# Performance work log

Hardware: AMD Instinct MI355X
Metric: run time of the kernel (lower is better)

Reference implementation:

```python
import jax, jax.numpy as jnp
import numpy as np

D_MODEL = 1024
NUM_HEADS = 16
HEAD_DIM = 64
INNER = NUM_HEADS * HEAD_DIM


def setup_inputs() -> dict:
    key = jax.random.key(0)
    k_x, k_q, k_k, k_v, k_o = jax.random.split(key, 5)
    B, T = 4, 2048
    s = 1.0 / np.sqrt(D_MODEL)
    return {
        "x": jax.random.normal(k_x, (B, T, D_MODEL), dtype=jnp.float32),
        "W_q": jax.random.uniform(k_q, (D_MODEL, INNER), dtype=jnp.float32, minval=-s, maxval=s),
        "W_k": jax.random.uniform(k_k, (D_MODEL, INNER), dtype=jnp.float32, minval=-s, maxval=s),
        "W_v": jax.random.uniform(k_v, (D_MODEL, INNER), dtype=jnp.float32, minval=-s, maxval=s),
        "W_o": jax.random.uniform(k_o, (INNER, D_MODEL), dtype=jnp.float32, minval=-s, maxval=s),
    }


def reference(x, W_q, W_k, W_v, W_o):
    B, T, _ = x.shape
    scale = HEAD_DIM ** -0.5
    # project and split heads: [B, H, T, Dh]
    q = (x @ W_q).reshape(B, T, NUM_HEADS, HEAD_DIM).transpose(0, 2, 1, 3)
    k = (x @ W_k).reshape(B, T, NUM_HEADS, HEAD_DIM).transpose(0, 2, 1, 3)
    v = (x @ W_v).reshape(B, T, NUM_HEADS, HEAD_DIM).transpose(0, 2, 1, 3)
    scores = jnp.einsum("bhqd,bhkd->bhqk", q, k) * scale  # [B,H,T,T]
    causal = jnp.tril(jnp.ones((T, T), dtype=bool))
    scores = jnp.where(causal, scores, -jnp.inf)
    probs = jax.nn.softmax(scores, axis=-1)
    ctx = jnp.einsum("bhqk,bhkd->bhqd", probs, v)
    ctx = ctx.transpose(0, 2, 1, 3).reshape(B, T, INNER)
    return ctx @ W_o
```

## Files before the change

### kernel.cpp

```cpp
#include <hip/hip_runtime.h>


typedef short  short8  __attribute__((ext_vector_type(8)));
typedef short  short4v __attribute__((ext_vector_type(4)));
typedef float  floatx4 __attribute__((ext_vector_type(4)));
typedef unsigned uint2v __attribute__((ext_vector_type(2)));

#define T_SZ 2048
#define DM   1024

#define QSCALE 0.18033688011112042f

__device__ __forceinline__ short f2bf(float f) {
  unsigned u = __float_as_uint(f);
  u += 0x7fffu + ((u >> 16) & 1u);
  return (short)(u >> 16);
}

#if defined(__has_builtin) && __has_builtin(__builtin_amdgcn_cvt_pk_bf16_f32)
typedef __bf16 bf16x2_t __attribute__((ext_vector_type(2)));
__device__ __forceinline__ unsigned pack_bf(float lo, float hi) {
  return __builtin_bit_cast(unsigned, __builtin_amdgcn_cvt_pk_bf16_f32(lo, hi));
}
#else
__device__ __forceinline__ unsigned pack_bf(float lo, float hi) {
  return __builtin_amdgcn_perm(__float_as_uint(hi) + 0x8000u,
                               __float_as_uint(lo) + 0x8000u, 0x07060302u);
}
#endif

#if defined(__has_builtin) && __has_builtin(__builtin_amdgcn_exp2f)
__device__ __forceinline__ float fexp2(float x) { return __builtin_amdgcn_exp2f(x); }
#else
__device__ __forceinline__ float fexp2(float x) { return exp2f(x); }
#endif

__device__ __forceinline__ void gll16(const void* g, void* l) {
  __builtin_amdgcn_global_load_lds((const __attribute__((address_space(1))) void*)g,
                                   (__attribute__((address_space(3))) void*)l, 16, 0, 0);
}

__global__ void cvt_kernel(const float* __restrict__ s0, const float* __restrict__ s1,
                           const float* __restrict__ s2, const float* __restrict__ s3,
                           short* __restrict__ dst,
                           const float* __restrict__ x, short* __restrict__ xb) {
  const int tx = threadIdx.x, ty = threadIdx.y;
  if (blockIdx.z == 4) {
    const int tid = ty * 32 + tx;
    const int blk = blockIdx.y * 32 + blockIdx.x;
    int i = (blk * 256 + tid) * 4;
#pragma unroll
    for (int j = 0; j < 8; ++j) {
      const float4 v = *(const float4*)(x + i);
      short4v o;
      o.x = f2bf(v.x); o.y = f2bf(v.y); o.z = f2bf(v.z); o.w = f2bf(v.w);
      *(short4v*)(xb + i) = o;
      i += 1048576;
    }
    return;
  }
  const float* srcs[4] = {s0, s1, s2, s3};
  const float* src = srcs[blockIdx.z];
  short* d = dst + (size_t)blockIdx.z * 1048576;
  __shared__ float tile[32][33];
  const int n_base = blockIdx.x * 32, k_base = blockIdx.y * 32;
#pragma unroll
  for (int j = 0; j < 4; ++j)
    tile[ty + j * 8][tx] = src[(size_t)(k_base + ty + j * 8) * 1024 + n_base + tx];
  __syncthreads();
#pragma unroll
  for (int j = 0; j < 4; ++j)
    d[(size_t)(n_base + ty + j * 8) * 1024 + k_base + tx] = f2bf(tile[tx][ty + j * 8]);
}

template <int MODE>
__global__ void gemm_bt(const short* __restrict__ A, const short* __restrict__ Bt,
                        short* __restrict__ obf, short* __restrict__ vt,
                        float* __restrict__ of, int K) {
  __shared__ short As[128 * 32];
  __shared__ short Bs[128 * 32];
  const int tid  = threadIdx.x;
  const int w    = tid >> 6, lane = tid & 63;
  const int quad = lane >> 4, l15 = lane & 15;
  const int wr   = w >> 1, wc = w & 1;
  const int lid  = (int)blockIdx.y * 64 + (int)blockIdx.x;
  const int m0   = (((lid & 7) + 8 * ((lid >> 3) & 7))) * 128;
  const int n0   = (lid >> 6) * 128;
  const int arow = tid >> 2, apart = tid & 3;

  floatx4 acc[4][4] = {};

  for (int kk = 0; kk < K; kk += 32) {
    gll16(A  + (size_t)(m0 + arow) * K      + kk + apart * 8, &As[tid * 8]);
    gll16(A  + (size_t)(m0 + 64 + arow) * K + kk + apart * 8, &As[(256 + tid) * 8]);
    gll16(Bt + (size_t)(n0 + arow) * K      + kk + apart * 8, &Bs[tid * 8]);
    gll16(Bt + (size_t)(n0 + 64 + arow) * K + kk + apart * 8, &Bs[(256 + tid) * 8]);
    __syncthreads();
    short8 af[4], bf[4];
#pragma unroll
    for (int i = 0; i < 4; ++i)
      af[i] = *(const short8*)&As[(wr * 64 + i * 16 + l15) * 32 + quad * 8];
#pragma unroll
    for (int j = 0; j < 4; ++j)
      bf[j] = *(const short8*)&Bs[(wc * 64 + j * 16 + l15) * 32 + quad * 8];
#pragma unroll
    for (int i = 0; i < 4; ++i)
#pragma unroll
      for (int j = 0; j < 4; ++j)
        acc[i][j] = __builtin_amdgcn_mfma_f32_16x16x32_bf16(af[i], bf[j], acc[i][j], 0, 0, 0);
    __syncthreads();
  }

  if (MODE == 0) {
    const int wsel = n0 >> 10;
    const int ncol0 = (n0 & 1023) + wc * 64;
    if (wsel < 2) {
      const float scale = (wsel == 0) ? QSCALE : 1.0f;
      short* outw = obf + (size_t)wsel * (64u * 2048u * 64u);
#pragma unroll
      for (int i = 0; i < 4; ++i) {
        const int row0 = m0 + wr * 64 + i * 16 + quad * 4;
#pragma unroll
        for (int j = 0; j < 4; ++j) {
          const int col = ncol0 + j * 16 + l15;
          const int h = col >> 6, d = col & 63;
#pragma unroll
          for (int r = 0; r < 4; ++r) {
            const int rg = row0 + r;
            const int b = rg >> 11, t = rg & 2047;
            outw[(((size_t)(b * 16 + h) * 2048 + t) << 6) + d] = f2bf(acc[i][j][r] * scale);
          }
        }
      }
    } else {
#pragma unroll
      for (int i = 0; i < 4; ++i) {
        const int row0 = m0 + wr * 64 + i * 16 + quad * 4;
        const int b = row0 >> 11, t = row0 & 2047;
#pragma unroll
        for (int j = 0; j < 4; ++j) {
          const int col = ncol0 + j * 16 + l15;
          const int h = col >> 6, d = col & 63;
          short4v pv;
#pragma unroll
          for (int r = 0; r < 4; ++r) pv[r] = f2bf(acc[i][j][r]);
          *(short4v*)(vt + (((size_t)(b * 16 + h) * 64 + d) << 11) + t) = pv;
        }
      }
    }
  } else {
#pragma unroll
    for (int i = 0; i < 4; ++i) {
      const int row0 = m0 + wr * 64 + i * 16 + quad * 4;
#pragma unroll
      for (int j = 0; j < 4; ++j) {
        const int col = n0 + wc * 64 + j * 16 + l15;
#pragma unroll
        for (int r = 0; r < 4; ++r)
          of[(size_t)(row0 + r) * 1024 + col] = acc[i][j][r];
      }
    }
  }
}

__global__ __launch_bounds__(256, 2) void attn_kernel(
    const short* __restrict__ Qg, const short* __restrict__ Kg,
    const short* __restrict__ Vt, short* __restrict__ ctx) {
  __shared__ short Ks[128 * 72];
  __shared__ short Vs[80 * 132];
  __shared__ short Ps[4 * 32 * 136];

  const int tid  = threadIdx.x;
  const int w    = tid >> 6, lane = tid & 63;
  const int quad = lane >> 4, l15 = lane & 15;
  const int bh = (int)blockIdx.x + 8 * ((int)blockIdx.y & 7);
  const int p  = (int)blockIdx.y >> 3;
  const int b  = bh >> 4, h = bh & 15;

  const size_t base = (size_t)bh * (T_SZ * 64);
  const short* Qb  = Qg + base;
  const short* Kb  = Kg + base;
  const short* Vtb = Vt + base;
  short* Pw = &Ps[w * (32 * 136)];

  const int skr = tid >> 1, skc = (tid & 1) * 32;
  const int svr = tid >> 2, svc = (tid & 3) * 32;

  {
    const int rr = 64 + (tid >> 4), cb = (tid & 15) * 8;
    const short vv = (tid < 16) ? (short)0x3F80 : (short)0;
    short8 fill;
#pragma unroll
    for (int j = 0; j < 8; ++j) fill[j] = vv;
    *(short8*)&Vs[rr * 132 + cb] = fill;
  }

  for (int qsel = 0; qsel < 2; ++qsel) {
    const int qi = qsel ? (15 - p) : p;
    const int q0 = qi << 7;
    const int rowA = q0 + w * 32;
    const int rowB = rowA + 16;

    const short8 qA0 = *(const short8*)(Qb + (size_t)(rowA + l15) * 64 + quad * 8);
    const short8 qA1 = *(const short8*)(Qb + (size_t)(rowA + l15) * 64 + 32 + quad * 8);
    const short8 qB0 = *(const short8*)(Qb + (size_t)(rowB + l15) * 64 + quad * 8);
    const short8 qB1 = *(const short8*)(Qb + (size_t)(rowB + l15) * 64 + 32 + quad * 8);

    floatx4 OA[4] = {}, OB[4] = {};
    floatx4 O5A = {}, O5B = {};

    const int ktiles = qi + 1;
    short8 kR[4], vR[4];
#pragma unroll
    for (int j = 0; j < 4; ++j) {
      kR[j] = *(const short8*)(Kb + (size_t)skr * 64 + skc + j * 8);
      vR[j] = *(const short8*)(Vtb + (size_t)svr * 2048 + svc + j * 8);
    }

    for (int kt = 0; kt < ktiles; ++kt) {
      const int k0 = kt << 7;
      __syncthreads();
#pragma unroll
      for (int j = 0; j < 4; ++j) {
        *(short8*)&Ks[skr * 72 + skc + j * 8] = kR[j];
        *(short8*)&Vs[svr * 132 + svc + j * 8] = vR[j];
      }
      if (kt + 1 < ktiles) {
        const int kn = (kt + 1) << 7;
#pragma unroll
        for (int j = 0; j < 4; ++j) {
          kR[j] = *(const short8*)(Kb + (size_t)(kn + skr) * 64 + skc + j * 8);
          vR[j] = *(const short8*)(Vtb + (size_t)svr * 2048 + kn + svc + j * 8);
        }
      }
      __syncthreads();

      const int dkA = rowA - k0;
      const int dkB = dkA + 16;
      const int limA = dkA + l15, limB = limA + 16;
      const int naA = min(8, (dkA >> 4) + 1), nchA = (naA + 1) >> 1;
      const int naB = min(8, (dkB >> 4) + 1), nchB = (naB + 1) >> 1;

#pragma unroll
      for (int mt = 0; mt < 8; ++mt) {
        const int pa = l15 * 136 + mt * 16 + quad * 4;
        const int pb = (16 + l15) * 136 + mt * 16 + quad * 4;
        const bool actA = (mt * 16 < dkA + 16);
        const bool actB = (mt * 16 < dkB + 16);
        if (actB) {
          const short8 kf0 = *(const short8*)&Ks[(mt * 16 + l15) * 72 + quad * 8];
          const short8 kf1 = *(const short8*)&Ks[(mt * 16 + l15) * 72 + 32 + quad * 8];
          {
            floatx4 s = {};
            s = __builtin_amdgcn_mfma_f32_16x16x32_bf16(kf0, qB0, s, 0, 0, 0);
            s = __builtin_amdgcn_mfma_f32_16x16x32_bf16(kf1, qB1, s, 0, 0, 0);
            if (mt * 16 + 15 > dkB) {
#pragma unroll
              for (int r = 0; r < 4; ++r)
                if (mt * 16 + quad * 4 + r > limB) s[r] = -1e30f;
            }
            floatx4 e;
#pragma unroll
            for (int r = 0; r < 4; ++r) e[r] = fexp2(s[r]);
            uint2v pd;
            pd.x = pack_bf(e[0], e[1]);
            pd.y = pack_bf(e[2], e[3]);
            *(uint2v*)&Pw[pb] = pd;
          }
          if (actA) {
            floatx4 s = {};
            s = __builtin_amdgcn_mfma_f32_16x16x32_bf16(kf0, qA0, s, 0, 0, 0);
            s = __builtin_amdgcn_mfma_f32_16x16x32_bf16(kf1, qA1, s, 0, 0, 0);
            if (mt * 16 + 15 > dkA) {
#pragma unroll
              for (int r = 0; r < 4; ++r)
                if (mt * 16 + quad * 4 + r > limA) s[r] = -1e30f;
            }
            floatx4 e;
#pragma unroll
            for (int r = 0; r < 4; ++r) e[r] = fexp2(s[r]);
            uint2v pd;
            pd.x = pack_bf(e[0], e[1]);
            pd.y = pack_bf(e[2], e[3]);
            *(uint2v*)&Pw[pa] = pd;
          } else if (mt < 2 * nchA) {
            uint2v z; z.x = 0; z.y = 0;
            *(uint2v*)&Pw[pa] = z;
          }
        } else {
          uint2v z; z.x = 0; z.y = 0;
          if (mt < 2 * nchB) *(uint2v*)&Pw[pb] = z;
          if (mt < 2 * nchA) *(uint2v*)&Pw[pa] = z;
        }
      }

#pragma unroll
      for (int c = 0; c < 4; ++c) {
        if (c < nchB) {
          const short8 vfl = *(const short8*)&Vs[(64 + l15) * 132 + c * 32 + quad * 8];
          short8 vf[4];
#pragma unroll
          for (int dt = 0; dt < 4; ++dt)
            vf[dt] = *(const short8*)&Vs[(dt * 16 + l15) * 132 + c * 32 + quad * 8];
          const short8 pfB = *(const short8*)&Pw[(16 + l15) * 136 + c * 32 + quad * 8];
#pragma unroll
          for (int dt = 0; dt < 4; ++dt)
            OB[dt] = __builtin_amdgcn_mfma_f32_16x16x32_bf16(vf[dt], pfB, OB[dt], 0, 0, 0);
          O5B = __builtin_amdgcn_mfma_f32_16x16x32_bf16(vfl, pfB, O5B, 0, 0, 0);
          if (c < nchA) {
            const short8 pfA = *(const short8*)&Pw[l15 * 136 + c * 32 + quad * 8];
#pragma unroll
            for (int dt = 0; dt < 4; ++dt)
              OA[dt] = __builtin_amdgcn_mfma_f32_16x16x32_bf16(vf[dt], pfA, OA[dt], 0, 0, 0);
            O5A = __builtin_amdgcn_mfma_f32_16x16x32_bf16(vfl, pfA, O5A, 0, 0, 0);
          }
        }
      }
    }

    {
      const float lA = __shfl(O5A[0], l15);
      const float invA = 1.0f / lA;
      const int t = rowA + l15;
      short* cb = ctx + (((size_t)(b * T_SZ + t)) << 10) + h * 64 + quad * 4;
#pragma unroll
      for (int dt = 0; dt < 4; ++dt) {
        short4v o4;
#pragma unroll
        for (int r = 0; r < 4; ++r) o4[r] = f2bf(OA[dt][r] * invA);
        *(short4v*)(cb + dt * 16) = o4;
      }
    }
    {
      const float lB = __shfl(O5B[0], l15);
      const float invB = 1.0f / lB;
      const int t = rowB + l15;
      short* cb = ctx + (((size_t)(b * T_SZ + t)) << 10) + h * 64 + quad * 4;
#pragma unroll
      for (int dt = 0; dt < 4; ++dt) {
        short4v o4;
#pragma unroll
        for (int r = 0; r < 4; ++r) o4[r] = f2bf(OB[dt][r] * invB);
        *(short4v*)(cb + dt * 16) = o4;
      }
    }
  }
}

extern "C" void kernel_launch(void* const* d_in, const int* in_sizes, int n_in,
                              void* d_out, int out_size, void* d_ws, size_t ws_size,
                              hipStream_t stream) {
  const float* x  = (const float*)d_in[0];
  const float* Wq = (const float*)d_in[1];
  const float* Wk = (const float*)d_in[2];
  const float* Wv = (const float*)d_in[3];
  const float* Wo = (const float*)d_in[4];
  float* out = (float*)d_out;

  short* ws  = (short*)d_ws;
  short* xb  = ws;
  short* Wt  = ws + 8388608;
  short* Qb  = Wt + 4 * 1048576;
  short* Kb  = Qb + 8388608;
  short* Vt  = Kb + 8388608;
  short* ctx = xb;

  cvt_kernel<<<dim3(32, 32, 5), dim3(32, 8), 0, stream>>>(Wq, Wk, Wv, Wo, Wt, x, xb);
  gemm_bt<0><<<dim3(64, 24), 256, 0, stream>>>(xb, Wt, Qb, Vt, nullptr, 1024);
  attn_kernel<<<dim3(8, 64), 256, 0, stream>>>(Qb, Kb, Vt, ctx);
  gemm_bt<1><<<dim3(64, 8), 256, 0, stream>>>(ctx, Wt + 3 * 1048576, nullptr, nullptr, out, 1024);
}
```

Measured before the change: 256.6 us.

## Add 256x256-tile pipelined QKV GEMM with swizzled LDS and double buffering

Replaces the generic 128x128 single-buffered QKV projection GEMM with a dedicated 512-thread kernel using 256x256 tiles, a BK=64 double-buffered LDS pipeline fed by direct global-to-LDS loads, XOR-swizzled LDS layout, and interleaved MFMA quadrants with manual waitcnt/barrier and setprio scheduling. It aims to cut global traffic through larger reuse, hide load latency behind MFMAs, and avoid LDS bank conflicts. The 128KB of LDS per block and fewer blocks (384) reduce occupancy, and the hand-written waitcnt sequencing risks subtle races.

```diff
diff --git a/kernel.cpp b/kernel.cpp
--- a/kernel.cpp
+++ b/kernel.cpp
@@ -39,6 +39,11 @@
   __builtin_amdgcn_global_load_lds((const __attribute__((address_space(1))) void*)g,
                                    (__attribute__((address_space(3))) void*)l, 16, 0, 0);
 }
+
+#define SBAR() asm volatile("s_barrier" ::: "memory")
+#define WLG()  asm volatile("s_waitcnt lgkmcnt(0)" ::: "memory")
+#define WV6()  asm volatile("s_waitcnt vmcnt(6)" ::: "memory")
+#define WV0()  asm volatile("s_waitcnt vmcnt(0)" ::: "memory")
 
 __global__ void cvt_kernel(const float* __restrict__ s0, const float* __restrict__ s1,
                            const float* __restrict__ s2, const float* __restrict__ s3,
@@ -71,6 +76,139 @@
 #pragma unroll
   for (int j = 0; j < 4; ++j)
     d[(size_t)(n_base + ty + j * 8) * 1024 + k_base + tx] = f2bf(tile[tx][ty + j * 8]);
+}
+
+__global__ __launch_bounds__(512, 2) void gemm_qkv(
+    const short* __restrict__ A, const short* __restrict__ Bt,
+    short* __restrict__ obf, short* __restrict__ vt) {
+  __shared__ short As[32768];
+  __shared__ short Bs[32768];
+  const int tid  = threadIdx.x;
+  const int w    = tid >> 6, lane = tid & 63;
+  const int quad = lane >> 4, l15 = lane & 15;
+  const int wr   = w >> 2, wc = w & 3;
+  const int fx   = l15 & 7;
+  const int lid  = (int)blockIdx.x;
+  const int m0   = ((lid & 7) * 4 + ((lid >> 3) & 3)) * 256;
+  const int n0   = (lid >> 5) * 256;
+  const int srow = tid >> 3;
+  const int scol = ((tid & 7) ^ (srow & 7)) * 8;
+
+  const short* Ag = A  + (size_t)(m0 + srow) * 1024 + scol;
+  const short* Bg = Bt + (size_t)(n0 + srow) * 1024 + scol;
+  const short* Ab[2] = { &As[(0 * 2 + wr) * 8192], &As[(1 * 2 + wr) * 8192] };
+  const short* Bb[2] = { &Bs[(0 * 2 + (wc >> 1)) * 8192], &Bs[(1 * 2 + (wc >> 1)) * 8192] };
+  const int br0 = (wc & 1) * 64;
+
+  floatx4 acc[8][4] = {};
+  short8 af[4][2], bf[4][2];
+
+#define STG_A(slot, h, kb) do { \
+    short* _lb = &As[((slot) * 2 + (h)) * 8192 + tid * 8]; \
+    const short* _gp = Ag + (size_t)(h) * (128 * 1024) + (kb); \
+    gll16(_gp, _lb); \
+    gll16(_gp + (size_t)(64 * 1024), _lb + 4096); \
+  } while (0)
+#define STG_B(slot, h, kb) do { \
+    short* _lb = &Bs[((slot) * 2 + (h)) * 8192 + tid * 8]; \
+    const short* _gp = Bg + (size_t)(h) * (128 * 1024) + (kb); \
+    gll16(_gp, _lb); \
+    gll16(_gp + (size_t)(64 * 1024), _lb + 4096); \
+  } while (0)
+#define LDA4(slot, ih) do { \
+    _Pragma("unroll") for (int ii = 0; ii < 4; ++ii) \
+    _Pragma("unroll") for (int s = 0; s < 2; ++s) \
+      af[ii][s] = *(const short8*)&Ab[slot][(((ih) * 4 + ii) * 16 + l15) * 64 + (((s * 4 + quad) ^ fx)) * 8]; \
+  } while (0)
+#define LDB8(slot) do { \
+    _Pragma("unroll") for (int j = 0; j < 4; ++j) \
+    _Pragma("unroll") for (int s = 0; s < 2; ++s) \
+      bf[j][s] = *(const short8*)&Bb[slot][(br0 + j * 16 + l15) * 64 + (((s * 4 + quad) ^ fx)) * 8]; \
+  } while (0)
+#define MMQ(ih, jh) do { \
+    __builtin_amdgcn_s_setprio(1); \
+    _Pragma("unroll") for (int ii = 0; ii < 4; ++ii) \
+    _Pragma("unroll") for (int jj = 0; jj < 2; ++jj) \
+    _Pragma("unroll") for (int s = 0; s < 2; ++s) \
+      acc[(ih) * 4 + ii][(jh) * 2 + jj] = __builtin_amdgcn_mfma_f32_16x16x32_bf16( \
+          af[ii][s], bf[(jh) * 2 + jj][s], acc[(ih) * 4 + ii][(jh) * 2 + jj], 0, 0, 0); \
+    __builtin_amdgcn_s_setprio(0); \
+  } while (0)
+
+  STG_A(0, 0, 0);  STG_A(0, 1, 0);
+  STG_B(0, 0, 0);  STG_B(0, 1, 0);
+  STG_B(1, 0, 64); STG_B(1, 1, 64);
+  STG_A(1, 0, 64);
+  WV6(); SBAR();
+
+  for (int t = 0; t < 8; ++t) {
+    const int kp1 = (2 * t + 1) * 64;
+    const int kn2 = (2 * t + 2) * 64;
+    const int kn3 = (2 * t + 3) * 64;
+    const bool mre = (t < 7);
+    LDA4(0, 0); LDB8(0);
+    STG_A(1, 1, kp1);
+    SBAR(); WLG(); MMQ(0, 0); SBAR();
+    if (mre) STG_B(0, 0, kn2);
+    SBAR(); MMQ(0, 1); SBAR();
+    LDA4(0, 1);
+    if (mre) STG_B(0, 1, kn2);
+    SBAR(); WLG(); MMQ(1, 0); SBAR();
+    if (mre) { STG_A(0, 0, kn2); WV6(); } else { WV0(); }
+    SBAR(); MMQ(1, 1); SBAR();
+    LDA4(1, 0); LDB8(1);
+    if (mre) STG_A(0, 1, kn2);
+    SBAR(); WLG(); MMQ(0, 0); SBAR();
+    if (mre) STG_B(1, 0, kn3);
+    SBAR(); MMQ(0, 1); SBAR();
+    LDA4(1, 1);
+    if (mre) STG_B(1, 1, kn3);
+    SBAR(); WLG(); MMQ(1, 0); SBAR();
+    if (mre) { STG_A(1, 0, kn3); WV6(); }
+    SBAR(); MMQ(1, 1); SBAR();
+  }
+
+  const int wsel  = n0 >> 10;
+  const int ncol0 = (n0 & 1023) + wc * 64;
+  if (wsel < 2) {
+    const float scale = (wsel == 0) ? QSCALE : 1.0f;
+    short* outw = obf + (size_t)wsel * (64u * 2048u * 64u);
+#pragma unroll
+    for (int i = 0; i < 8; ++i) {
+      const int row0 = m0 + wr * 128 + i * 16 + quad * 4;
+#pragma unroll
+      for (int j = 0; j < 4; ++j) {
+        const int col = ncol0 + j * 16 + l15;
+        const int h = col >> 6, d = col & 63;
+#pragma unroll
+        for (int r = 0; r < 4; ++r) {
+          const int rg = row0 + r;
+          const int b = rg >> 11, tt = rg & 2047;
+          outw[(((size_t)(b * 16 + h) * 2048 + tt) << 6) + d] = f2bf(acc[i][j][r] * scale);
+        }
+      }
+    }
+  } else {
+#pragma unroll
+    for (int i = 0; i < 8; ++i) {
+      const int row0 = m0 + wr * 128 + i * 16 + quad * 4;
+      const int b = row0 >> 11, tt = row0 & 2047;
+#pragma unroll
+      for (int j = 0; j < 4; ++j) {
+        const int col = ncol0 + j * 16 + l15;
+        const int h = col >> 6, d = col & 63;
+        short4v pv;
+#pragma unroll
+        for (int r = 0; r < 4; ++r) pv[r] = f2bf(acc[i][j][r]);
+        *(short4v*)(vt + (((size_t)(b * 16 + h) * 64 + d) << 11) + tt) = pv;
+      }
+    }
+  }
+#undef STG_A
+#undef STG_B
+#undef LDA4
+#undef LDB8
+#undef MMQ
 }
 
 template <int MODE>
@@ -96,18 +234,18 @@
     gll16(Bt + (size_t)(n0 + arow) * K      + kk + apart * 8, &Bs[tid * 8]);
     gll16(Bt + (size_t)(n0 + 64 + arow) * K + kk + apart * 8, &Bs[(256 + tid) * 8]);
     __syncthreads();
-    short8 af[4], bf[4];
+    short8 af[4], bfr[4];
 #pragma unroll
     for (int i = 0; i < 4; ++i)
       af[i] = *(const short8*)&As[(wr * 64 + i * 16 + l15) * 32 + quad * 8];
 #pragma unroll
     for (int j = 0; j < 4; ++j)
-      bf[j] = *(const short8*)&Bs[(wc * 64 + j * 16 + l15) * 32 + quad * 8];
+      bfr[j] = *(const short8*)&Bs[(wc * 64 + j * 16 + l15) * 32 + quad * 8];
 #pragma unroll
     for (int i = 0; i < 4; ++i)
 #pragma unroll
       for (int j = 0; j < 4; ++j)
-        acc[i][j] = __builtin_amdgcn_mfma_f32_16x16x32_bf16(af[i], bf[j], acc[i][j], 0, 0, 0);
+        acc[i][j] = __builtin_amdgcn_mfma_f32_16x16x32_bf16(af[i], bfr[j], acc[i][j], 0, 0, 0);
     __syncthreads();
   }
 
@@ -366,7 +504,7 @@
   short* ctx = xb;
 
   cvt_kernel<<<dim3(32, 32, 5), dim3(32, 8), 0, stream>>>(Wq, Wk, Wv, Wo, Wt, x, xb);
-  gemm_bt<0><<<dim3(64, 24), 256, 0, stream>>>(xb, Wt, Qb, Vt, nullptr, 1024);
+  gemm_qkv<<<dim3(384), 512, 0, stream>>>(xb, Wt, Qb, Vt);
   attn_kernel<<<dim3(8, 64), 256, 0, stream>>>(Qb, Kb, Vt, ctx);
   gemm_bt<1><<<dim3(64, 8), 256, 0, stream>>>(ctx, Wt + 3 * 1048576, nullptr, nullptr, out, 1024);
 }
```

Result: slower. 264.8 us (+3.2%).

## Restructure attention into 512-thread blocks over 256-row query tiles with chunked P

Applied to the files above, without the earlier changes.

The attention kernel now launches 512 threads (8 waves) per block. Each block covers one 256-row query tile, where before it processed two 128-row tiles in sequence to balance causal work. The tile order is reversed so the heaviest tiles start first. The probability scratch shrinks to a per-chunk 32x32 buffer per wave, with QK^T/exp and PV interleaved per 32-key chunk. Waves whose rows are entirely above the current key tile skip compute but still take part in the loads and barriers. This raises parallelism per block and lowers LDS use, but leaves some waves idle in the early key tiles.

```diff
diff --git a/kernel.cpp b/kernel.cpp
--- a/kernel.cpp
+++ b/kernel.cpp
@@ -96,18 +96,18 @@
     gll16(Bt + (size_t)(n0 + arow) * K      + kk + apart * 8, &Bs[tid * 8]);
     gll16(Bt + (size_t)(n0 + 64 + arow) * K + kk + apart * 8, &Bs[(256 + tid) * 8]);
     __syncthreads();
-    short8 af[4], bf[4];
+    short8 af[4], bfr[4];
 #pragma unroll
     for (int i = 0; i < 4; ++i)
       af[i] = *(const short8*)&As[(wr * 64 + i * 16 + l15) * 32 + quad * 8];
 #pragma unroll
     for (int j = 0; j < 4; ++j)
-      bf[j] = *(const short8*)&Bs[(wc * 64 + j * 16 + l15) * 32 + quad * 8];
+      bfr[j] = *(const short8*)&Bs[(wc * 64 + j * 16 + l15) * 32 + quad * 8];
 #pragma unroll
     for (int i = 0; i < 4; ++i)
 #pragma unroll
       for (int j = 0; j < 4; ++j)
-        acc[i][j] = __builtin_amdgcn_mfma_f32_16x16x32_bf16(af[i], bf[j], acc[i][j], 0, 0, 0);
+        acc[i][j] = __builtin_amdgcn_mfma_f32_16x16x32_bf16(af[i], bfr[j], acc[i][j], 0, 0, 0);
     __syncthreads();
   }
 
@@ -163,186 +163,184 @@
   }
 }
 
-__global__ __launch_bounds__(256, 2) void attn_kernel(
+__global__ __launch_bounds__(512, 4) void attn_kernel(
     const short* __restrict__ Qg, const short* __restrict__ Kg,
     const short* __restrict__ Vt, short* __restrict__ ctx) {
   __shared__ short Ks[128 * 72];
-  __shared__ short Vs[80 * 132];
-  __shared__ short Ps[4 * 32 * 136];
+  __shared__ short Vs[80 * 136];
+  __shared__ short Ps[8 * 32 * 40];
 
   const int tid  = threadIdx.x;
   const int w    = tid >> 6, lane = tid & 63;
   const int quad = lane >> 4, l15 = lane & 15;
   const int bh = (int)blockIdx.x + 8 * ((int)blockIdx.y & 7);
-  const int p  = (int)blockIdx.y >> 3;
+  const int g  = (int)blockIdx.y >> 3;
+  const int qb = (g < 4) ? (7 - g) : (g - 4);
   const int b  = bh >> 4, h = bh & 15;
 
   const size_t base = (size_t)bh * (T_SZ * 64);
   const short* Qb  = Qg + base;
   const short* Kb  = Kg + base;
   const short* Vtb = Vt + base;
-  short* Pw = &Ps[w * (32 * 136)];
-
-  const int skr = tid >> 1, skc = (tid & 1) * 32;
-  const int svr = tid >> 2, svc = (tid & 3) * 32;
-
-  {
+  short* Pw = &Ps[w * 1280];
+
+  const int skr = tid >> 2, skp = (tid & 3) * 16;
+  const int svr = tid >> 3, svp = (tid & 7) * 16;
+
+  if (tid < 256) {
     const int rr = 64 + (tid >> 4), cb = (tid & 15) * 8;
     const short vv = (tid < 16) ? (short)0x3F80 : (short)0;
     short8 fill;
 #pragma unroll
     for (int j = 0; j < 8; ++j) fill[j] = vv;
-    *(short8*)&Vs[rr * 132 + cb] = fill;
-  }
-
-  for (int qsel = 0; qsel < 2; ++qsel) {
-    const int qi = qsel ? (15 - p) : p;
-    const int q0 = qi << 7;
-    const int rowA = q0 + w * 32;
-    const int rowB = rowA + 16;
-
-    const short8 qA0 = *(const short8*)(Qb + (size_t)(rowA + l15) * 64 + quad * 8);
-    const short8 qA1 = *(const short8*)(Qb + (size_t)(rowA + l15) * 64 + 32 + quad * 8);
-    const short8 qB0 = *(const short8*)(Qb + (size_t)(rowB + l15) * 64 + quad * 8);
-    const short8 qB1 = *(const short8*)(Qb + (size_t)(rowB + l15) * 64 + 32 + quad * 8);
-
-    floatx4 OA[4] = {}, OB[4] = {};
-    floatx4 O5A = {}, O5B = {};
-
-    const int ktiles = qi + 1;
-    short8 kR[4], vR[4];
-#pragma unroll
-    for (int j = 0; j < 4; ++j) {
-      kR[j] = *(const short8*)(Kb + (size_t)skr * 64 + skc + j * 8);
-      vR[j] = *(const short8*)(Vtb + (size_t)svr * 2048 + svc + j * 8);
-    }
-
-    for (int kt = 0; kt < ktiles; ++kt) {
-      const int k0 = kt << 7;
-      __syncthreads();
-#pragma unroll
-      for (int j = 0; j < 4; ++j) {
-        *(short8*)&Ks[skr * 72 + skc + j * 8] = kR[j];
-        *(short8*)&Vs[svr * 132 + svc + j * 8] = vR[j];
-      }
-      if (kt + 1 < ktiles) {
-        const int kn = (kt + 1) << 7;
-#pragma unroll
-        for (int j = 0; j < 4; ++j) {
-          kR[j] = *(const short8*)(Kb + (size_t)(kn + skr) * 64 + skc + j * 8);
-          vR[j] = *(const short8*)(Vtb + (size_t)svr * 2048 + kn + svc + j * 8);
+    *(short8*)&Vs[rr * 136 + cb] = fill;
+  }
+
+  const int rowA = qb * 256 + w * 32;
+  const int rowB = rowA + 16;
+  const int ktmax = 2 * qb + 2;
+
+  const short8 qA0 = *(const short8*)(Qb + (size_t)(rowA + l15) * 64 + quad * 8);
+  const short8 qA1 = *(const short8*)(Qb + (size_t)(rowA + l15) * 64 + 32 + quad * 8);
+  const short8 qB0 = *(const short8*)(Qb + (size_t)(rowB + l15) * 64 + quad * 8);
+  const short8 qB1 = *(const short8*)(Qb + (size_t)(rowB + l15) * 64 + 32 + quad * 8);
+
+  floatx4 OA[4] = {}, OB[4] = {};
+  floatx4 O5A = {}, O5B = {};
+
+  short8 kR[2], vR[2];
+  kR[0] = *(const short8*)(Kb + (size_t)skr * 64 + skp);
+  kR[1] = *(const short8*)(Kb + (size_t)skr * 64 + skp + 8);
+  vR[0] = *(const short8*)(Vtb + (size_t)svr * 2048 + svp);
+  vR[1] = *(const short8*)(Vtb + (size_t)svr * 2048 + svp + 8);
+
+  for (int kt = 0; kt < ktmax; ++kt) {
+    const int k0 = kt << 7;
+    __syncthreads();
+    *(short8*)&Ks[skr * 72 + skp]     = kR[0];
+    *(short8*)&Ks[skr * 72 + skp + 8] = kR[1];
+    *(short8*)&Vs[svr * 136 + svp]     = vR[0];
+    *(short8*)&Vs[svr * 136 + svp + 8] = vR[1];
+    if (kt + 1 < ktmax) {
+      const int kn = (kt + 1) << 7;
+      kR[0] = *(const short8*)(Kb + (size_t)(kn + skr) * 64 + skp);
+      kR[1] = *(const short8*)(Kb + (size_t)(kn + skr) * 64 + skp + 8);
+      vR[0] = *(const short8*)(Vtb + (size_t)svr * 2048 + kn + svp);
+      vR[1] = *(const short8*)(Vtb + (size_t)svr * 2048 + kn + svp + 8);
+    }
+    __syncthreads();
+
+    const int dkA = rowA - k0;
+    if (dkA < 0) continue;
+    const int dkB = dkA + 16;
+    const int limA = dkA + l15, limB = limA + 16;
+    const int naA = min(8, (dkA >> 4) + 1), nchA = (naA + 1) >> 1;
+    const int naB = min(8, (dkB >> 4) + 1), nchB = (naB + 1) >> 1;
+
+#pragma unroll
+    for (int c = 0; c < 4; ++c) {
+      if (c < nchB) {
+#pragma unroll
+        for (int mm = 0; mm < 2; ++mm) {
+          const int mt = 2 * c + mm;
+          const int pa = l15 * 40 + mm * 16 + quad * 4;
+          const int pb = (16 + l15) * 40 + mm * 16 + quad * 4;
+          const bool aB = (mt * 16 < dkB + 16);
+          const bool aA = (mt * 16 < dkA + 16);
+          if (aB) {
+            const short8 kf0 = *(const short8*)&Ks[(mt * 16 + l15) * 72 + quad * 8];
+            const short8 kf1 = *(const short8*)&Ks[(mt * 16 + l15) * 72 + 32 + quad * 8];
+            {
+              floatx4 s = {};
+              s = __builtin_amdgcn_mfma_f32_16x16x32_bf16(kf0, qB0, s, 0, 0, 0);
+              s = __builtin_amdgcn_mfma_f32_16x16x32_bf16(kf1, qB1, s, 0, 0, 0);
+              if (mt * 16 + 15 > dkB) {
+#pragma unroll
+                for (int r = 0; r < 4; ++r)
+                  if (mt * 16 + quad * 4 + r > limB) s[r] = -1e30f;
+              }
+              floatx4 e;
+#pragma unroll
+              for (int r = 0; r < 4; ++r) e[r] = fexp2(s[r]);
+              uint2v pd;
+              pd.x = pack_bf(e[0], e[1]);
+              pd.y = pack_bf(e[2], e[3]);
+              *(uint2v*)&Pw[pb] = pd;
+            }
+            if (c < nchA) {
+              if (aA) {
+                floatx4 s = {};
+                s = __builtin_amdgcn_mfma_f32_16x16x32_bf16(kf0, qA0, s, 0, 0, 0);
+                s = __builtin_amdgcn_mfma_f32_16x16x32_bf16(kf1, qA1, s, 0, 0, 0);
+                if (mt * 16 + 15 > dkA) {
+#pragma unroll
+                  for (int r = 0; r < 4; ++r)
+                    if (mt * 16 + quad * 4 + r > limA) s[r] = -1e30f;
+                }
+                floatx4 e;
+#pragma unroll
+                for (int r = 0; r < 4; ++r) e[r] = fexp2(s[r]);
+                uint2v pd;
+                pd.x = pack_bf(e[0], e[1]);
+                pd.y = pack_bf(e[2], e[3]);
+                *(uint2v*)&Pw[pa] = pd;
+              } else {
+                uint2v z; z.x = 0; z.y = 0;
+                *(uint2v*)&Pw[pa] = z;
+              }
+            }
+          } else {
+            uint2v z; z.x = 0; z.y = 0;
+            *(uint2v*)&Pw[pb] = z;
+            if (c < nchA) *(uint2v*)&Pw[pa] = z;
+          }
+        }
+        const int vcol = c * 32 + quad * 8;
+        const short8 vfl = *(const short8*)&Vs[(64 + l15) * 136 + vcol];
+        short8 vf[4];
+#pragma unroll
+        for (int dt = 0; dt < 4; ++dt)
+          vf[dt] = *(const short8*)&Vs[(dt * 16 + l15) * 136 + vcol];
+        const short8 pfB = *(const short8*)&Pw[(16 + l15) * 40 + quad * 8];
+#pragma unroll
+        for (int dt = 0; dt < 4; ++dt)
+          OB[dt] = __builtin_amdgcn_mfma_f32_16x16x32_bf16(vf[dt], pfB, OB[dt], 0, 0, 0);
+        O5B = __builtin_amdgcn_mfma_f32_16x16x32_bf16(vfl, pfB, O5B, 0, 0, 0);
+        if (c < nchA) {
+          const short8 pfA = *(const short8*)&Pw[l15 * 40 + quad * 8];
+#pragma unroll
+          for (int dt = 0; dt < 4; ++dt)
+            OA[dt] = __builtin_amdgcn_mfma_f32_16x16x32_bf16(vf[dt], pfA, OA[dt], 0, 0, 0);
+          O5A = __builtin_amdgcn_mfma_f32_16x16x32_bf16(vfl, pfA, O5A, 0, 0, 0);
         }
       }
-      __syncthreads();
-
-      const int dkA = rowA - k0;
-      const int dkB = dkA + 16;
-      const int limA = dkA + l15, limB = limA + 16;
-      const int naA = min(8, (dkA >> 4) + 1), nchA = (naA + 1) >> 1;
-      const int naB = min(8, (dkB >> 4) + 1), nchB = (naB + 1) >> 1;
-
-#pragma unroll
-      for (int mt = 0; mt < 8; ++mt) {
-        const int pa = l15 * 136 + mt * 16 + quad * 4;
-        const int pb = (16 + l15) * 136 + mt * 16 + quad * 4;
-        const bool actA = (mt * 16 < dkA + 16);
-        const bool actB = (mt * 16 < dkB + 16);
-        if (actB) {
-          const short8 kf0 = *(const short8*)&Ks[(mt * 16 + l15) * 72 + quad * 8];
-          const short8 kf1 = *(const short8*)&Ks[(mt * 16 + l15) * 72 + 32 + quad * 8];
-          {
-            floatx4 s = {};
-            s = __builtin_amdgcn_mfma_f32_16x16x32_bf16(kf0, qB0, s, 0, 0, 0);
-            s = __builtin_amdgcn_mfma_f32_16x16x32_bf16(kf1, qB1, s, 0, 0, 0);
-            if (mt * 16 + 15 > dkB) {
-#pragma unroll
-              for (int r = 0; r < 4; ++r)
-                if (mt * 16 + quad * 4 + r > limB) s[r] = -1e30f;
-            }
-            floatx4 e;
-#pragma unroll
-            for (int r = 0; r < 4; ++r) e[r] = fexp2(s[r]);
-            uint2v pd;
-            pd.x = pack_bf(e[0], e[1]);
-            pd.y = pack_bf(e[2], e[3]);
-            *(uint2v*)&Pw[pb] = pd;
-          }
-          if (actA) {
-            floatx4 s = {};
-            s = __builtin_amdgcn_mfma_f32_16x16x32_bf16(kf0, qA0, s, 0, 0, 0);
-            s = __builtin_amdgcn_mfma_f32_16x16x32_bf16(kf1, qA1, s, 0, 0, 0);
-            if (mt * 16 + 15 > dkA) {
-#pragma unroll
-              for (int r = 0; r < 4; ++r)
-                if (mt * 16 + quad * 4 + r > limA) s[r] = -1e30f;
-            }
-            floatx4 e;
-#pragma unroll
-            for (int r = 0; r < 4; ++r) e[r] = fexp2(s[r]);
-            uint2v pd;
-            pd.x = pack_bf(e[0], e[1]);
-            pd.y = pack_bf(e[2], e[3]);
-            *(uint2v*)&Pw[pa] = pd;
-          } else if (mt < 2 * nchA) {
-            uint2v z; z.x = 0; z.y = 0;
-            *(uint2v*)&Pw[pa] = z;
-          }
-        } else {
-          uint2v z; z.x = 0; z.y = 0;
-          if (mt < 2 * nchB) *(uint2v*)&Pw[pb] = z;
-          if (mt < 2 * nchA) *(uint2v*)&Pw[pa] = z;
-        }
-      }
-
-#pragma unroll
-      for (int c = 0; c < 4; ++c) {
-        if (c < nchB) {
-          const short8 vfl = *(const short8*)&Vs[(64 + l15) * 132 + c * 32 + quad * 8];
-          short8 vf[4];
-#pragma unroll
-          for (int dt = 0; dt < 4; ++dt)
-            vf[dt] = *(const short8*)&Vs[(dt * 16 + l15) * 132 + c * 32 + quad * 8];
-          const short8 pfB = *(const short8*)&Pw[(16 + l15) * 136 + c * 32 + quad * 8];
-#pragma unroll
-          for (int dt = 0; dt < 4; ++dt)
-            OB[dt] = __builtin_amdgcn_mfma_f32_16x16x32_bf16(vf[dt], pfB, OB[dt], 0, 0, 0);
-          O5B = __builtin_amdgcn_mfma_f32_16x16x32_bf16(vfl, pfB, O5B, 0, 0, 0);
-          if (c < nchA) {
-            const short8 pfA = *(const short8*)&Pw[l15 * 136 + c * 32 + quad * 8];
-#pragma unroll
-            for (int dt = 0; dt < 4; ++dt)
-              OA[dt] = __builtin_amdgcn_mfma_f32_16x16x32_bf16(vf[dt], pfA, OA[dt], 0, 0, 0);
-            O5A = __builtin_amdgcn_mfma_f32_16x16x32_bf16(vfl, pfA, O5A, 0, 0, 0);
-          }
-        }
-      }
-    }
-
-    {
-      const float lA = __shfl(O5A[0], l15);
-      const float invA = 1.0f / lA;
-      const int t = rowA + l15;
-      short* cb = ctx + (((size_t)(b * T_SZ + t)) << 10) + h * 64 + quad * 4;
-#pragma unroll
-      for (int dt = 0; dt < 4; ++dt) {
-        short4v o4;
-#pragma unroll
-        for (int r = 0; r < 4; ++r) o4[r] = f2bf(OA[dt][r] * invA);
-        *(short4v*)(cb + dt * 16) = o4;
-      }
-    }
-    {
-      const float lB = __shfl(O5B[0], l15);
-      const float invB = 1.0f / lB;
-      const int t = rowB + l15;
-      short* cb = ctx + (((size_t)(b * T_SZ + t)) << 10) + h * 64 + quad * 4;
-#pragma unroll
-      for (int dt = 0; dt < 4; ++dt) {
-        short4v o4;
-#pragma unroll
-        for (int r = 0; r < 4; ++r) o4[r] = f2bf(OB[dt][r] * invB);
-        *(short4v*)(cb + dt * 16) = o4;
-      }
+    }
+  }
+
+  {
+    const float lA = __shfl(O5A[0], l15);
+    const float invA = 1.0f / lA;
+    const int t = rowA + l15;
+    short* cb = ctx + (((size_t)(b * T_SZ + t)) << 10) + h * 64 + quad * 4;
+#pragma unroll
+    for (int dt = 0; dt < 4; ++dt) {
+      short4v o4;
+#pragma unroll
+      for (int r = 0; r < 4; ++r) o4[r] = f2bf(OA[dt][r] * invA);
+      *(short4v*)(cb + dt * 16) = o4;
+    }
+  }
+  {
+    const float lB = __shfl(O5B[0], l15);
+    const float invB = 1.0f / lB;
+    const int t = rowB + l15;
+    short* cb = ctx + (((size_t)(b * T_SZ + t)) << 10) + h * 64 + quad * 4;
+#pragma unroll
+    for (int dt = 0; dt < 4; ++dt) {
+      short4v o4;
+#pragma unroll
+      for (int r = 0; r < 4; ++r) o4[r] = f2bf(OB[dt][r] * invB);
+      *(short4v*)(cb + dt * 16) = o4;
     }
   }
 }
@@ -367,6 +365,6 @@
 
   cvt_kernel<<<dim3(32, 32, 5), dim3(32, 8), 0, stream>>>(Wq, Wk, Wv, Wo, Wt, x, xb);
   gemm_bt<0><<<dim3(64, 24), 256, 0, stream>>>(xb, Wt, Qb, Vt, nullptr, 1024);
-  attn_kernel<<<dim3(8, 64), 256, 0, stream>>>(Qb, Kb, Vt, ctx);
+  attn_kernel<<<dim3(8, 64), 512, 0, stream>>>(Qb, Kb, Vt, ctx);
   gemm_bt<1><<<dim3(64, 8), 256, 0, stream>>>(ctx, Wt + 3 * 1048576, nullptr, nullptr, out, 1024);
 }
```

Result: faster. 242.8 us (-5.4%).
